# Kernel optimization log

Hardware: AMD Instinct MI355X
Metric: run time of the kernel (lower is better)

Reference implementation:

```python
import jax, jax.numpy as jnp
import numpy as np

WS = 4        # window_size
SS = 2        # shift_size
NH = 8        # num_heads
EPS = 1e-5    # LayerNorm eps (torch default)


def _rel_pos_index(ws):
    coords = np.stack(np.meshgrid(np.arange(ws), np.arange(ws), indexing='ij')).reshape(2, -1)
    rel = (coords[:, :, None] - coords[:, None, :]).transpose(1, 2, 0)
    rel[..., 0] += ws - 1
    rel[..., 1] += ws - 1
    rel[..., 0] *= 2 * ws - 1
    return rel.sum(-1)  # [N, N] ints

REL_IDX = _rel_pos_index(WS)


def _shift_mask(Hp, Wp, ws, ss):
    # standard Swin shifted-window region mask: 0 within region, -100 across regions
    img = np.zeros((Hp, Wp))
    cnt = 0
    for hs in (slice(0, -ws), slice(-ws, -ss), slice(-ss, None)):
        for wsl in (slice(0, -ws), slice(-ws, -ss), slice(-ss, None)):
            img[hs, wsl] = cnt
            cnt += 1
    mw = img.reshape(Hp // ws, ws, Wp // ws, ws).transpose(0, 2, 1, 3).reshape(-1, ws * ws)
    d = mw[:, None, :] - mw[:, :, None]
    return np.where(d != 0, -100.0, 0.0).astype(np.float32)  # [nW, N, N]


def _ln(x, g, b):
    m = jnp.mean(x, -1, keepdims=True)
    v = jnp.mean((x - m) ** 2, -1, keepdims=True)
    return (x - m) * jax.lax.rsqrt(v + EPS) * g + b


def setup_inputs() -> dict:
    key = jax.random.key(0)
    ks = jax.random.split(key, 8)
    D, F = 512, 1024
    rn = lambda k, s: (jax.random.normal(k, s, jnp.float32) * 0.02)
    return {
        'x': jax.random.normal(ks[0], (4, 64 * 128, D), jnp.float32),
        'g1': jnp.ones((D,), jnp.float32), 'beta1': jnp.zeros((D,), jnp.float32),
        'w_qkv': rn(ks[1], (3 * D, D)), 'b_qkv': jnp.zeros((3 * D,), jnp.float32),
        'rpb': rn(ks[2], ((2 * WS - 1) ** 2, NH)),
        'w_proj': rn(ks[3], (D, D)), 'b_proj': jnp.zeros((D,), jnp.float32),
        'g2': jnp.ones((D,), jnp.float32), 'beta2': jnp.zeros((D,), jnp.float32),
        'w1': rn(ks[4], (F, D)), 'b1': jnp.zeros((F,), jnp.float32),
        'w2': rn(ks[5], (D, F)), 'b2': jnp.zeros((D,), jnp.float32),
        'H': 64, 'W': 128,
    }


def reference(x, g1, beta1, w_qkv, b_qkv, rpb, w_proj, b_proj, g2, beta2, w1, b1, w2, b2, H, W):
    B, L, C = x.shape
    hd = C // NH
    scale = hd ** (-0.5)
    N = WS * WS
    Hp, Wp = H, W  # H, W chosen divisible by WS -> no padding branch
    nW = (Hp // WS) * (Wp // WS)

    shortcut = x
    h = _ln(x, g1, beta1).reshape(B, H, W, C)
    # cyclic shift
    h = jnp.roll(h, (-SS, -SS), axis=(1, 2))
    # window partition -> [B*nW, N, C]
    xw = h.reshape(B, Hp // WS, WS, Wp // WS, WS, C).transpose(0, 1, 3, 2, 4, 5).reshape(-1, N, C)

    qkv = (xw @ w_qkv.T + b_qkv).reshape(-1, N, 3, NH, hd).transpose(2, 0, 3, 1, 4)
    q, k, v = qkv[0] * scale, qkv[1], qkv[2]          # [B*nW, NH, N, hd]
    attn = jnp.einsum('whnd,whmd->whnm', q, k)        # [B*nW, NH, N, N]

    bias = rpb[REL_IDX.reshape(-1)].reshape(N, N, NH).transpose(2, 0, 1)  # [NH, N, N]
    attn = attn + bias[None]

    mask = jnp.asarray(_shift_mask(Hp, Wp, WS, SS))   # [nW, N, N]
    attn = attn.reshape(B, nW, NH, N, N) + mask[None, :, None]
    attn = jax.nn.softmax(attn.reshape(-1, NH, N, N), axis=-1)

    o = jnp.einsum('whnm,whmd->whnd', attn, v).transpose(0, 2, 1, 3).reshape(-1, N, C)
    o = o @ w_proj.T + b_proj
    # window reverse + reverse shift
    o = o.reshape(B, Hp // WS, Wp // WS, WS, WS, C).transpose(0, 1, 3, 2, 4, 5).reshape(B, Hp, Wp, C)
    o = jnp.roll(o, (SS, SS), axis=(1, 2)).reshape(B, H * W, C)

    x = shortcut + o
    h2 = _ln(x, g2, beta2)
    m = jax.nn.gelu(h2 @ w1.T + b1, approximate=False) @ w2.T + b2
    return x + m
```

## Files before the change

kernel.cpp:

```cpp
#include <hip/hip_runtime.h>
#include <hip/hip_bf16.h>
#include <math.h>

typedef __bf16 bf16_t;
typedef __bf16 bf16x8 __attribute__((ext_vector_type(8)));
typedef float f32x4 __attribute__((ext_vector_type(4)));


#define X1_OFF   0u
#define XW_OFF   67108864u
#define QKV_OFF  100663296u
#define WQ_OFF   201326592u
#define WP_OFF   202899456u
#define W1_OFF   203423744u
#define W2_OFF   204472320u
#define SV_OFF   205520896u
#define FLAG_OFF 205545472u

__device__ __forceinline__ int perm_row(int r) {
    int b   = r >> 13;
    int rem = r & 8191;
    int w   = rem >> 4;
    int n   = rem & 15;
    int wy  = w >> 5, wx = w & 31;
    int y   = wy * 4 + (n >> 2);
    int x   = wx * 4 + (n & 3);
    int ys  = (y + 2) & 63;
    int xs  = (x + 2) & 127;
    return (b << 13) + (ys << 7) + xs;
}

__device__ __forceinline__ void gld16(const void* g, void* l) {
    __builtin_amdgcn_global_load_lds(
        (const __attribute__((address_space(1))) unsigned int*)(unsigned long long)(uintptr_t)g,
        (__attribute__((address_space(3))) unsigned int*)(unsigned int)(uintptr_t)l,
        16, 0, 0);
}

#define SBAR __builtin_amdgcn_sched_barrier(0)
#define BARRIER do { SBAR; __builtin_amdgcn_s_barrier(); SBAR; } while (0)

__global__ __launch_bounds__(256) void k_probe(const unsigned short* __restrict__ x,
                                               int n, int* __restrict__ flag) {
    __shared__ int cnt;
    if (threadIdx.x == 0) cnt = 0;
    __syncthreads();
    int c = 0;
    for (int i = threadIdx.x; i < n; i += 256) {
        int e = (x[i] >> 7) & 0xFF;
        if (e >= 0xC0) c++;
    }
    atomicAdd(&cnt, c);
    __syncthreads();
    if (threadIdx.x == 0) *flag = (cnt > 8) ? 1 : 0;
}

__global__ __launch_bounds__(256) void k_cvt_bf16(const void* __restrict__ src,
                                                  bf16_t* __restrict__ dst, int n,
                                                  const int* __restrict__ flag) {
    int i = blockIdx.x * 256 + threadIdx.x;
    if (i >= n) return;
    dst[i] = (*flag) ? (bf16_t)((const float*)src)[i] : ((const bf16_t*)src)[i];
}

__global__ __launch_bounds__(256) void k_cvt_small(
        const void* g1, const void* be1, const void* bq, const void* bp,
        const void* g2, const void* be2, const void* b1, const void* b2,
        const void* rpb, float* __restrict__ dst, const int* __restrict__ flag) {
    int i = blockIdx.x * 256 + threadIdx.x;
    const void* src; int off;
    if      (i < 512)  { src = g1;  off = i; }
    else if (i < 1024) { src = be1; off = i - 512; }
    else if (i < 2560) { src = bq;  off = i - 1024; }
    else if (i < 3072) { src = bp;  off = i - 2560; }
    else if (i < 3584) { src = g2;  off = i - 3072; }
    else if (i < 4096) { src = be2; off = i - 3584; }
    else if (i < 5120) { src = b1;  off = i - 4096; }
    else if (i < 5632) { src = b2;  off = i - 5120; }
    else if (i < 6024) { src = rpb; off = i - 5632; }
    else return;
    dst[i] = (*flag) ? ((const float*)src)[off] : (float)((const bf16_t*)src)[off];
}

__global__ __launch_bounds__(256) void k_ln1(const void* __restrict__ x,
                                             const float* __restrict__ g,
                                             const float* __restrict__ be,
                                             bf16_t* __restrict__ xw,
                                             const int* __restrict__ flag) {
    int r    = blockIdx.x * 4 + (threadIdx.x >> 6);
    int lane = threadIdx.x & 63;
    int f    = *flag;
    long ro  = (long)perm_row(r) * 512;
    const float*  x32 = (const float*)x + ro;
    const bf16_t* x16 = (const bf16_t*)x + ro;
    int base = lane * 8;
    float v[8];
    float s = 0.f, ss = 0.f;
#pragma unroll
    for (int j = 0; j < 8; j++) {
        float t = f ? x32[base + j] : (float)x16[base + j];
        v[j] = t; s += t; ss += t * t;
    }
#pragma unroll
    for (int off = 32; off; off >>= 1) {
        s  += __shfl_down(s,  off, 64);
        ss += __shfl_down(ss, off, 64);
    }
    s  = __shfl(s, 0, 64);
    ss = __shfl(ss, 0, 64);
    float m   = s * (1.f / 512.f);
    float var = ss * (1.f / 512.f) - m * m;
    float inv = rsqrtf(var + 1e-5f);
    bf16_t* orow = xw + (long)r * 512;
#pragma unroll
    for (int j = 0; j < 8; j++)
        orow[base + j] = (bf16_t)((v[j] - m) * inv * g[base + j] + be[base + j]);
}

__global__ __launch_bounds__(256) void k_ln2(const float* __restrict__ x1,
                                             const float* __restrict__ g,
                                             const float* __restrict__ be,
                                             bf16_t* __restrict__ h2) {
    int r    = blockIdx.x * 4 + (threadIdx.x >> 6);
    int lane = threadIdx.x & 63;
    const float* xr = x1 + (long)r * 512;
    int base = lane * 8;
    float v[8];
    float s = 0.f, ss = 0.f;
#pragma unroll
    for (int j = 0; j < 8; j++) {
        float t = xr[base + j];
        v[j] = t; s += t; ss += t * t;
    }
#pragma unroll
    for (int off = 32; off; off >>= 1) {
        s  += __shfl_down(s,  off, 64);
        ss += __shfl_down(ss, off, 64);
    }
    s  = __shfl(s, 0, 64);
    ss = __shfl(ss, 0, 64);
    float m   = s * (1.f / 512.f);
    float var = ss * (1.f / 512.f) - m * m;
    float inv = rsqrtf(var + 1e-5f);
    bf16_t* orow = h2 + (long)r * 512;
#pragma unroll
    for (int j = 0; j < 8; j++)
        orow[base + j] = (bf16_t)((v[j] - m) * inv * g[base + j] + be[base + j]);
}

template<int EPI>
__global__ __launch_bounds__(512, 2) void k_gemm256(const bf16_t* __restrict__ A,
                                                    const bf16_t* __restrict__ Wt,
                                                    const float* __restrict__ bias,
                                                    void* __restrict__ out,
                                                    const void* __restrict__ res,
                                                    const int* __restrict__ flag,
                                                    int N, int K) {
    __shared__ __attribute__((aligned(16))) char smem[131072];
    int tid  = threadIdx.x;
    int lane = tid & 63, wv = tid >> 6;

    int nbx = N >> 8;
    int id  = blockIdx.x;
    int xb  = (id >> 3) % nbx;
    int yb  = ((id >> 3) / nbx) * 8 + (id & 7);
    int m0  = yb << 8, n0 = xb << 8;

    int srow = tid >> 3;
    int cg   = (tid & 7) ^ (srow & 7);
    const bf16_t* gA = A  + (long)(m0 + srow) * K + cg * 8;
    const bf16_t* gB = Wt + (long)(n0 + srow) * K + cg * 8;
    long r64 = (long)64 * K;

    int rr = lane & 15, quad = lane >> 4;
    int wh = wv >> 2, wq = wv & 3;
    int lA  = (wh * 64 + rr) * 128;
    int lB  = (wq * 32 + rr) * 128;
    int ck0 = (quad ^ (rr & 7)) * 16;
    int ck1 = ck0 ^ 64;

    f32x4 acc[8][4];
#pragma unroll
    for (int mi = 0; mi < 8; mi++)
#pragma unroll
        for (int ni = 0; ni < 4; ni++) { f32x4 z = {0.f,0.f,0.f,0.f}; acc[mi][ni] = z; }

    int S = K >> 6;

    gld16(gA,             smem + 0     + wv * 1024);
    gld16(gA + r64,       smem + 8192  + wv * 1024);
    gld16(gB,             smem + 32768 + wv * 1024);
    gld16(gB + r64,       smem + 40960 + wv * 1024);
    gld16(gB + 2 * r64,   smem + 49152 + wv * 1024);
    gld16(gB + 3 * r64,   smem + 57344 + wv * 1024);
    gld16(gA + 2 * r64,   smem + 16384 + wv * 1024);
    gld16(gA + 3 * r64,   smem + 24576 + wv * 1024);

    bf16x8 af[4][2], bg[2][2];

#define DO_PHASE(AH, BH, LOADA)                                               \
    do {                                                                      \
        if (LOADA) {                                                          \
            _Pragma("unroll") for (int mi = 0; mi < 4; mi++) {                \
                af[mi][0] = *(const bf16x8*)(bc + (AH)*16384 + lA + mi*2048 + ck0); \
                af[mi][1] = *(const bf16x8*)(bc + (AH)*16384 + lA + mi*2048 + ck1); \
            }                                                                 \
        }                                                                     \
        _Pragma("unroll") for (int ni = 0; ni < 2; ni++) {                    \
            bg[ni][0] = *(const bf16x8*)(bc + 32768 + (BH)*16384 + lB + ni*2048 + ck0); \
            bg[ni][1] = *(const bf16x8*)(bc + 32768 + (BH)*16384 + lB + ni*2048 + ck1); \
        }                                                                     \
        asm volatile("s_waitcnt lgkmcnt(0)" ::: "memory"); SBAR;              \
        __builtin_amdgcn_s_setprio(1);                                        \
        _Pragma("unroll") for (int mi = 0; mi < 4; mi++)                      \
            _Pragma("unroll") for (int ni = 0; ni < 2; ni++)                  \
                _Pragma("unroll") for (int kk = 0; kk < 2; kk++)              \
                    acc[(AH)*4 + mi][(BH)*2 + ni] =                           \
                        __builtin_amdgcn_mfma_f32_16x16x32_bf16(              \
                            af[mi][kk], bg[ni][kk], acc[(AH)*4 + mi][(BH)*2 + ni], 0, 0, 0); \
        __builtin_amdgcn_s_setprio(0);                                        \
    } while (0)

#define STAGE(GP, SLOT)                                                       \
    do { gld16((GP) + kn,       bn + (SLOT) + wv * 1024);                     \
         gld16((GP) + r64 + kn, bn + (SLOT) + 8192 + wv * 1024); } while (0)

    for (int t = 0; t < S - 1; ++t) {
        char* bc = smem + (t & 1) * 65536;
        char* bn = smem + ((t & 1) ^ 1) * 65536;
        long  kn = (long)(t + 1) * 64;
        STAGE(gA, 0);
        asm volatile("s_waitcnt vmcnt(6)" ::: "memory");
        BARRIER;
        DO_PHASE(0, 0, 1);
        BARRIER;
        STAGE(gB, 32768);
        asm volatile("s_waitcnt vmcnt(6)" ::: "memory");
        BARRIER;
        DO_PHASE(0, 1, 0);
        BARRIER;
        STAGE(gB + 2 * r64, 49152);
        asm volatile("s_waitcnt vmcnt(6)" ::: "memory");
        BARRIER;
        DO_PHASE(1, 0, 1);
        BARRIER;
        STAGE(gA + 2 * r64, 16384);
        DO_PHASE(1, 1, 0);
        BARRIER;
    }
    {
        char* bc = smem + ((S - 1) & 1) * 65536;
        asm volatile("s_waitcnt vmcnt(4)" ::: "memory");
        BARRIER;
        DO_PHASE(0, 0, 1);
        BARRIER;
        asm volatile("s_waitcnt vmcnt(2)" ::: "memory");
        BARRIER;
        DO_PHASE(0, 1, 0);
        BARRIER;
        asm volatile("s_waitcnt vmcnt(0)" ::: "memory");
        BARRIER;
        DO_PHASE(1, 0, 1);
        BARRIER;
        DO_PHASE(1, 1, 0);
        BARRIER;
    }
#undef DO_PHASE
#undef STAGE

    float* sc = (float*)(smem + wv * 16384);
    int f    = (EPI == 1 || EPI == 3) ? *flag : 0;
    int j8   = lane & 7;
    int rl   = lane >> 3;
    int colg = n0 + wq * 32 + (j8 >> 2) * 128 + ((j8 * 8) & 31);
    f32x4 b0 = *(const f32x4*)(bias + colg);
    f32x4 b1 = *(const f32x4*)(bias + colg + 4);

#pragma unroll
    for (int ah = 0; ah < 2; ++ah) {
#pragma unroll
        for (int bh = 0; bh < 2; ++bh)
#pragma unroll
            for (int ni = 0; ni < 2; ++ni)
#pragma unroll
                for (int mi = 0; mi < 4; ++mi)
#pragma unroll
                    for (int i = 0; i < 4; ++i) {
                        int r  = mi * 16 + quad * 4 + i;
                        int cl = bh * 32 + ni * 16 + rr;
                        sc[r * 64 + ((((cl >> 2) ^ (r & 15)) << 2) | (cl & 3))] =
                            acc[ah * 4 + mi][bh * 2 + ni][i];
                    }
#pragma unroll
        for (int p = 0; p < 8; ++p) {
            int r = p * 8 + rl;
            f32x4 v0 = *(const f32x4*)(sc + r * 64 + (((2 * j8)     ^ (r & 15)) << 2));
            f32x4 v1 = *(const f32x4*)(sc + r * 64 + (((2 * j8 + 1) ^ (r & 15)) << 2));
            int row = m0 + ah * 128 + wh * 64 + r;
            v0 += b0; v1 += b1;

            if (EPI == 0) {
                bf16x8 ob;
#pragma unroll
                for (int c = 0; c < 4; c++) { ob[c] = (bf16_t)v0[c]; ob[c + 4] = (bf16_t)v1[c]; }
                *(bf16x8*)((bf16_t*)out + (long)row * N + colg) = ob;
            } else if (EPI == 1) {
                long o = (long)perm_row(row) * 512 + colg;
                if (f) {
                    f32x4 r0 = *(const f32x4*)((const float*)res + o);
                    f32x4 r1 = *(const f32x4*)((const float*)res + o + 4);
                    v0 += r0; v1 += r1;
                } else {
                    bf16x8 rb = *(const bf16x8*)((const bf16_t*)res + o);
#pragma unroll
                    for (int c = 0; c < 4; c++) { v0[c] += (float)rb[c]; v1[c] += (float)rb[c + 4]; }
                }
                *(f32x4*)((float*)out + o)     = v0;
                *(f32x4*)((float*)out + o + 4) = v1;
            } else if (EPI == 2) {
                bf16x8 ob;
#pragma unroll
                for (int c = 0; c < 4; c++) {
                    float a0 = v0[c], a1 = v1[c];
                    ob[c]     = (bf16_t)(0.5f * a0 * (1.f + erff(a0 * 0.70710678118654752f)));
                    ob[c + 4] = (bf16_t)(0.5f * a1 * (1.f + erff(a1 * 0.70710678118654752f)));
                }
                *(bf16x8*)((bf16_t*)out + (long)row * N + colg) = ob;
            } else {
                long o = (long)row * 512 + colg;
                f32x4 r0 = *(const f32x4*)((const float*)res + o);
                f32x4 r1 = *(const f32x4*)((const float*)res + o + 4);
                v0 += r0; v1 += r1;
                if (f) {
                    *(f32x4*)((float*)out + o)     = v0;
                    *(f32x4*)((float*)out + o + 4) = v1;
                } else {
                    bf16x8 ob;
#pragma unroll
                    for (int c = 0; c < 4; c++) { ob[c] = (bf16_t)v0[c]; ob[c + 4] = (bf16_t)v1[c]; }
                    *(bf16x8*)((bf16_t*)out + o) = ob;
                }
            }
        }
    }
}

__global__ __launch_bounds__(256) void k_attn(const bf16_t* __restrict__ qkv,
                                              const float* __restrict__ rpb,
                                              bf16_t* __restrict__ O) {
    __shared__ float q[16][68], k[16][68], v[16][68];
    __shared__ float S[16][17];

    int blk = blockIdx.x;
    int h   = blk & 7;
    int w   = blk >> 3;
    int tid = threadIdx.x;

    int n0 = tid >> 4;
    int d0 = (tid & 15) * 4;
    const bf16_t* base = qkv + (long)(w * 16 + n0) * 1536 + h * 64 + d0;
#pragma unroll
    for (int j = 0; j < 4; j++) {
        q[n0][d0 + j] = (float)base[j] * 0.125f;
        k[n0][d0 + j] = (float)base[512 + j];
        v[n0][d0 + j] = (float)base[1024 + j];
    }
    __syncthreads();

    int i = tid >> 4, j = tid & 15;
    float s = 0.f;
#pragma unroll
    for (int d = 0; d < 64; d++) s += q[i][d] * k[j][d];

    int iy = i >> 2, ix = i & 3, jy = j >> 2, jx = j & 3;
    s += rpb[((iy - jy + 3) * 7 + (ix - jx + 3)) * 8 + h];

    int wl = w & 511;
    int wy = wl >> 5, wx = wl & 31;
    int yi = wy * 4 + iy, xi = wx * 4 + ix;
    int yj = wy * 4 + jy, xj = wx * 4 + jx;
    int ri = (yi < 60 ? 0 : (yi < 62 ? 1 : 2)) * 3 + (xi < 124 ? 0 : (xi < 126 ? 1 : 2));
    int rj = (yj < 60 ? 0 : (yj < 62 ? 1 : 2)) * 3 + (xj < 124 ? 0 : (xj < 126 ? 1 : 2));
    if (ri != rj) s -= 100.f;
    S[i][j] = s;
    __syncthreads();

    if (tid < 16) {
        float mx = -1e30f;
#pragma unroll
        for (int c = 0; c < 16; c++) mx = fmaxf(mx, S[tid][c]);
        float sum = 0.f;
#pragma unroll
        for (int c = 0; c < 16; c++) { float e = expf(S[tid][c] - mx); S[tid][c] = e; sum += e; }
        float invs = 1.f / sum;
#pragma unroll
        for (int c = 0; c < 16; c++) S[tid][c] *= invs;
    }
    __syncthreads();

#pragma unroll
    for (int t = 0; t < 4; t++) {
        int e  = tid + t * 256;
        int oi = e >> 6, od = e & 63;
        float acc = 0.f;
#pragma unroll
        for (int c = 0; c < 16; c++) acc += S[oi][c] * v[c][od];
        O[(long)(w * 16 + oi) * 512 + h * 64 + od] = (bf16_t)acc;
    }
}

extern "C" void kernel_launch(void* const* d_in, const int* in_sizes, int n_in,
                              void* d_out, int out_size, void* d_ws, size_t ws_size,
                              hipStream_t stream) {
    char* ws = (char*)d_ws;
    float*  x1   = (float*)(ws + X1_OFF);
    bf16_t* xw   = (bf16_t*)(ws + XW_OFF);
    bf16_t* qkv  = (bf16_t*)(ws + QKV_OFF);
    bf16_t* wq_b = (bf16_t*)(ws + WQ_OFF);
    bf16_t* wp_b = (bf16_t*)(ws + WP_OFF);
    bf16_t* w1_b = (bf16_t*)(ws + W1_OFF);
    bf16_t* w2_b = (bf16_t*)(ws + W2_OFF);
    float*  sv   = (float*)(ws + SV_OFF);
    int*    flag = (int*)(ws + FLAG_OFF);

    k_probe<<<1, 256, 0, stream>>>((const unsigned short*)d_in[0], 4096, flag);
    k_cvt_bf16<<<3072, 256, 0, stream>>>(d_in[3],  wq_b, 786432, flag);
    k_cvt_bf16<<<1024, 256, 0, stream>>>(d_in[6],  wp_b, 262144, flag);
    k_cvt_bf16<<<2048, 256, 0, stream>>>(d_in[10], w1_b, 524288, flag);
    k_cvt_bf16<<<2048, 256, 0, stream>>>(d_in[12], w2_b, 524288, flag);
    k_cvt_small<<<24,  256, 0, stream>>>(d_in[1], d_in[2], d_in[4], d_in[7],
                                         d_in[8], d_in[9], d_in[11], d_in[13],
                                         d_in[5], sv, flag);

    k_ln1<<<dim3(8192), dim3(256), 0, stream>>>(d_in[0], sv, sv + 512, xw, flag);
    k_gemm256<0><<<dim3(768), dim3(512), 0, stream>>>(xw, wq_b, sv + 1024, qkv, nullptr, flag, 1536, 512);
    k_attn<<<dim3(16384), dim3(256), 0, stream>>>(qkv, sv + 5632, xw );
    k_gemm256<1><<<dim3(256), dim3(512), 0, stream>>>(xw, wp_b, sv + 2560, x1, d_in[0], flag, 512, 512);
    k_ln2<<<dim3(8192), dim3(256), 0, stream>>>(x1, sv + 3072, sv + 3584, xw );
    k_gemm256<2><<<dim3(512), dim3(512), 0, stream>>>(xw, w1_b, sv + 4096, qkv , nullptr, flag, 1024, 512);
    k_gemm256<3><<<dim3(256), dim3(512), 0, stream>>>(qkv, w2_b, sv + 5120, d_out, x1, flag, 512, 1024);
}
```

Before: 442.0 us.

## Restructure GEMM main loop to issue LDS fragment loads before global staging

Rewrites the double-buffered GEMM K-loop so the LDS fragment reads for each quadrant are issued before the next global-to-LDS stage and its vmcnt wait. Barriers are reduced from two per phase to one. The separate tail iteration is folded into the loop behind a predicate. The aim is to overlap LDS reads with global-load latency and cut barrier stalls, at the cost of more complex wait-count bookkeeping and a possible race if the counts are wrong.

```diff
diff --git a/kernel.cpp b/kernel.cpp
--- a/kernel.cpp
+++ b/kernel.cpp
@@ -195,21 +195,23 @@
     gld16(gB + 3 * r64,   smem + 57344 + wv * 1024);
     gld16(gA + 2 * r64,   smem + 16384 + wv * 1024);
     gld16(gA + 3 * r64,   smem + 24576 + wv * 1024);
+    asm volatile("s_waitcnt vmcnt(4)" ::: "memory");
+    BARRIER;
 
     bf16x8 af[4][2], bg[2][2];
 
-#define DO_PHASE(AH, BH, LOADA)                                               \
+#define FRAG_A(AH)                                                            \
+    _Pragma("unroll") for (int mi = 0; mi < 4; mi++) {                        \
+        af[mi][0] = *(const bf16x8*)(bc + (AH)*16384 + lA + mi*2048 + ck0);   \
+        af[mi][1] = *(const bf16x8*)(bc + (AH)*16384 + lA + mi*2048 + ck1);   \
+    }
+#define FRAG_B(BH)                                                            \
+    _Pragma("unroll") for (int ni = 0; ni < 2; ni++) {                        \
+        bg[ni][0] = *(const bf16x8*)(bc + 32768 + (BH)*16384 + lB + ni*2048 + ck0); \
+        bg[ni][1] = *(const bf16x8*)(bc + 32768 + (BH)*16384 + lB + ni*2048 + ck1); \
+    }
+#define MFMA_CL(AH, BH)                                                       \
     do {                                                                      \
-        if (LOADA) {                                                          \
-            _Pragma("unroll") for (int mi = 0; mi < 4; mi++) {                \
-                af[mi][0] = *(const bf16x8*)(bc + (AH)*16384 + lA + mi*2048 + ck0); \
-                af[mi][1] = *(const bf16x8*)(bc + (AH)*16384 + lA + mi*2048 + ck1); \
-            }                                                                 \
-        }                                                                     \
-        _Pragma("unroll") for (int ni = 0; ni < 2; ni++) {                    \
-            bg[ni][0] = *(const bf16x8*)(bc + 32768 + (BH)*16384 + lB + ni*2048 + ck0); \
-            bg[ni][1] = *(const bf16x8*)(bc + 32768 + (BH)*16384 + lB + ni*2048 + ck1); \
-        }                                                                     \
         asm volatile("s_waitcnt lgkmcnt(0)" ::: "memory"); SBAR;              \
         __builtin_amdgcn_s_setprio(1);                                        \
         _Pragma("unroll") for (int mi = 0; mi < 4; mi++)                      \
@@ -220,52 +222,41 @@
                             af[mi][kk], bg[ni][kk], acc[(AH)*4 + mi][(BH)*2 + ni], 0, 0, 0); \
         __builtin_amdgcn_s_setprio(0);                                        \
     } while (0)
-
 #define STAGE(GP, SLOT)                                                       \
     do { gld16((GP) + kn,       bn + (SLOT) + wv * 1024);                     \
          gld16((GP) + r64 + kn, bn + (SLOT) + 8192 + wv * 1024); } while (0)
 
-    for (int t = 0; t < S - 1; ++t) {
+    for (int t = 0; t < S; ++t) {
         char* bc = smem + (t & 1) * 65536;
         char* bn = smem + ((t & 1) ^ 1) * 65536;
         long  kn = (long)(t + 1) * 64;
-        STAGE(gA, 0);
-        asm volatile("s_waitcnt vmcnt(6)" ::: "memory");
+        bool  st = (t + 1 < S);
+        FRAG_A(0); FRAG_B(0);
+        if (st) { STAGE(gA, 0);
+                  asm volatile("s_waitcnt vmcnt(4)" ::: "memory"); }
+        else    { asm volatile("s_waitcnt vmcnt(2)" ::: "memory"); }
         BARRIER;
-        DO_PHASE(0, 0, 1);
+        MFMA_CL(0, 0);
+        FRAG_B(1);
+        if (st) { STAGE(gB, 32768);
+                  asm volatile("s_waitcnt vmcnt(4)" ::: "memory"); }
+        else    { asm volatile("s_waitcnt vmcnt(0)" ::: "memory"); }
         BARRIER;
-        STAGE(gB, 32768);
-        asm volatile("s_waitcnt vmcnt(6)" ::: "memory");
+        MFMA_CL(0, 1);
+        FRAG_A(1); FRAG_B(0);
+        if (st) STAGE(gB + 2 * r64, 49152);
         BARRIER;
-        DO_PHASE(0, 1, 0);
+        MFMA_CL(1, 0);
+        FRAG_B(1);
+        if (st) { STAGE(gA + 2 * r64, 16384);
+                  asm volatile("s_waitcnt vmcnt(4)" ::: "memory"); }
         BARRIER;
-        STAGE(gB + 2 * r64, 49152);
-        asm volatile("s_waitcnt vmcnt(6)" ::: "memory");
-        BARRIER;
-        DO_PHASE(1, 0, 1);
-        BARRIER;
-        STAGE(gA + 2 * r64, 16384);
-        DO_PHASE(1, 1, 0);
-        BARRIER;
-    }
-    {
-        char* bc = smem + ((S - 1) & 1) * 65536;
-        asm volatile("s_waitcnt vmcnt(4)" ::: "memory");
-        BARRIER;
-        DO_PHASE(0, 0, 1);
-        BARRIER;
-        asm volatile("s_waitcnt vmcnt(2)" ::: "memory");
-        BARRIER;
-        DO_PHASE(0, 1, 0);
-        BARRIER;
-        asm volatile("s_waitcnt vmcnt(0)" ::: "memory");
-        BARRIER;
-        DO_PHASE(1, 0, 1);
-        BARRIER;
-        DO_PHASE(1, 1, 0);
-        BARRIER;
-    }
-#undef DO_PHASE
+        MFMA_CL(1, 1);
+    }
+    BARRIER;
+#undef FRAG_A
+#undef FRAG_B
+#undef MFMA_CL
 #undef STAGE
 
     float* sc = (float*)(smem + wv * 16384);
```

Result: slower. 453.3 us (+2.6%).
